# Kernel optimization log

Hardware: AMD Instinct MI355X
Metric: run time of the kernel (lower is better)

## Reference

```python
import jax, jax.numpy as jnp
import numpy as np

B, N_O, N_Q = 2, 512, 512
POS_DIM, LATENT, HEADS, HEAD_DIM, OUT_DIM = 3, 256, 8, 32, 128
HD = HEADS * HEAD_DIM  # == LATENT here


def _lin(key, fan_in, fan_out):
    return jax.random.normal(key, (fan_in, fan_out), jnp.float32) / np.sqrt(fan_in)


def setup_inputs() -> dict:
    key = jax.random.key(0)
    ks = jax.random.split(key, 12)
    return {
        'h_obs': jax.random.normal(ks[0], (B, N_O, LATENT), jnp.float32),
        'pos_obs': jax.random.uniform(ks[1], (B, N_O, POS_DIM), jnp.float32),
        'pos_query': jax.random.uniform(ks[2], (B, N_Q, POS_DIM), jnp.float32),
        'fw1': _lin(ks[3], LATENT, LATENT), 'fb1': jnp.zeros((LATENT,), jnp.float32),
        'fw2': _lin(ks[4], LATENT, HD), 'fb2': jnp.zeros((HD,), jnp.float32),
        'log_sigma': jnp.zeros((HEADS,), jnp.float32),
        'kw1': _lin(ks[5], POS_DIM * 3, LATENT), 'kb1': jnp.zeros((LATENT,), jnp.float32),
        'kw2': _lin(ks[6], LATENT, HEADS), 'kb2': jnp.zeros((HEADS,), jnp.float32),
        'ow': _lin(ks[7], HD, OUT_DIM), 'ob': jnp.zeros((OUT_DIM,), jnp.float32),
        'vw': _lin(ks[8], HD, OUT_DIM), 'vb': jnp.zeros((OUT_DIM,), jnp.float32),
    }


def reference(h_obs, pos_obs, pos_query, fw1, fb1, fw2, fb2, log_sigma,
              kw1, kb1, kw2, kb2, ow, ob, vw, vb):
    Bv, No, _ = h_obs.shape
    Nq = pos_query.shape[1]
    # feature net -> values [B, H, N_o, D]
    v = jax.nn.relu(h_obs @ fw1 + fb1) @ fw2 + fb2
    v = v.reshape(Bv, No, HEADS, HEAD_DIM).transpose(0, 2, 1, 3)
    # pairwise relative positions [B, Nq, No, P]
    pos_q = pos_query[:, :, None, :]
    pos_o = pos_obs[:, None, :, :]
    rel = pos_q - pos_o
    dist2 = jnp.sum(rel ** 2, axis=-1)  # [B, Nq, No]
    sigma = jnp.exp(log_sigma)[None, :, None, None]
    rbf = jnp.exp(-dist2[:, None] / (sigma ** 2 + 1e-6))  # [B, H, Nq, No]
    # kernel MLP on concatenated pairwise positions [B, Nq, No, 3P] -> [B, H, Nq, No]
    ki = jnp.concatenate([
        jnp.broadcast_to(pos_q, (Bv, Nq, No, POS_DIM)),
        jnp.broadcast_to(pos_o, (Bv, Nq, No, POS_DIM)),
        rel], axis=-1)
    delta = (jax.nn.relu(ki @ kw1 + kb1) @ kw2 + kb2).transpose(0, 3, 1, 2)
    logits = jnp.log(rbf + 1e-8) + delta
    weights = jax.nn.softmax(logits, axis=-1)  # [B, H, Nq, No]
    # weighted mean over observations
    v_mean = jnp.einsum('bhqo,bhod->bhqd', weights, v)  # [B, H, Nq, D]
    h_query = v_mean.transpose(0, 2, 1, 3).reshape(Bv, Nq, HD)
    # weighted variance: sum_o w * (v_o - v_mean)^2
    residual = v[:, :, None, :, :] - v_mean[:, :, :, None, :]  # [B, H, Nq, No, D]
    var = jnp.sum(weights[..., None] * residual ** 2, axis=3)  # [B, H, Nq, D]
    var = var.transpose(0, 2, 1, 3).reshape(Bv, Nq, HD)
    mean = h_query @ ow + ob
    var_out = jax.nn.softplus(var @ vw + vb)
    return (mean, var_out)
```

## Files before the change

kernel.cpp:

```cpp
#include <hip/hip_runtime.h>
#include <math.h>

#define NB 2
#define NO 512
#define NQ 512
#define OUT_DIM 128
#define LPAD 514

typedef __attribute__((ext_vector_type(8))) short short8;
typedef __attribute__((ext_vector_type(8))) _Float16 half8;
typedef __attribute__((ext_vector_type(4))) float f32x4;
typedef float v2f __attribute__((ext_vector_type(2)));

__device__ __forceinline__ float softplus_f(float x) {
  return x > 0.0f ? x + log1pf(expf(-x)) : log1pf(expf(x));
}
__device__ __forceinline__ unsigned short bf16_rne(float f) {
  unsigned u = __float_as_uint(f);
  unsigned r = u + 0x7FFFu + ((u >> 16) & 1u);
  return (unsigned short)(r >> 16);
}
__device__ __forceinline__ v2f unpk_bf2(unsigned u) {
  v2f r; r.x = __uint_as_float(u << 16); r.y = __uint_as_float(u & 0xFFFF0000u);
  return r;
}
__device__ __forceinline__ v2f splat2(float x) { v2f r; r.x = x; r.y = x; return r; }
__device__ __forceinline__ v2f fma2(v2f a, v2f b, v2f c) { return __builtin_elementwise_fma(a, b, c); }
__device__ __forceinline__ v2f max2(v2f a, v2f b) { return __builtin_elementwise_max(a, b); }
__device__ __forceinline__ int cvt2h(float x, float y) {
  return __builtin_bit_cast(int, __builtin_amdgcn_cvt_pkrtz(x, y));
}
__device__ __forceinline__ v2f bfly_s(v2f x) {
  #pragma unroll
  for (int off = 8; off <= 32; off <<= 1) {
    x.x += __shfl_xor(x.x, off, 64);
    x.y += __shfl_xor(x.y, off, 64);
  }
  return x;
}

__global__ __launch_bounds__(1024) void prep_kernel(
    const float* __restrict__ h_obs, const float* __restrict__ fw1,
    const float* __restrict__ fb1, const float* __restrict__ fw2,
    const float* __restrict__ fb2, const float* __restrict__ pos_obs,
    const float* __restrict__ kw1, unsigned short* __restrict__ V_bf,
    unsigned short* __restrict__ AO_bf)
{
  if (blockIdx.x < 256) {
    __shared__ float s_red[4][4][256];
    __shared__ float s_hid[4][256];
    const int n  = threadIdx.x & 255;
    const int ks = threadIdx.x >> 8;
    const int r0 = blockIdx.x * 4;
    const int k0 = ks * 64;
    float a0 = 0.f, a1 = 0.f, a2 = 0.f, a3 = 0.f;
    #pragma unroll 8
    for (int kk = 0; kk < 64; ++kk) {
      int k = k0 + kk;
      float w = fw1[k * 256 + n];
      a0 = fmaf(h_obs[(r0 + 0) * 256 + k], w, a0);
      a1 = fmaf(h_obs[(r0 + 1) * 256 + k], w, a1);
      a2 = fmaf(h_obs[(r0 + 2) * 256 + k], w, a2);
      a3 = fmaf(h_obs[(r0 + 3) * 256 + k], w, a3);
    }
    s_red[ks][0][n] = a0; s_red[ks][1][n] = a1;
    s_red[ks][2][n] = a2; s_red[ks][3][n] = a3;
    __syncthreads();
    if (ks == 0) {
      float bb = fb1[n];
      #pragma unroll
      for (int r = 0; r < 4; ++r) {
        float v = s_red[0][r][n] + s_red[1][r][n] + s_red[2][r][n] + s_red[3][r][n] + bb;
        s_hid[r][n] = fmaxf(v, 0.f);
      }
    }
    __syncthreads();
    float c0 = 0.f, c1 = 0.f, c2 = 0.f, c3 = 0.f;
    #pragma unroll 8
    for (int kk = 0; kk < 64; ++kk) {
      int k = k0 + kk;
      float w = fw2[k * 256 + n];
      c0 = fmaf(s_hid[0][k], w, c0);
      c1 = fmaf(s_hid[1][k], w, c1);
      c2 = fmaf(s_hid[2][k], w, c2);
      c3 = fmaf(s_hid[3][k], w, c3);
    }
    __syncthreads();
    s_red[ks][0][n] = c0; s_red[ks][1][n] = c1;
    s_red[ks][2][n] = c2; s_red[ks][3][n] = c3;
    __syncthreads();
    if (ks == 0) {
      float bb = fb2[n];
      #pragma unroll
      for (int r = 0; r < 4; ++r) {
        float v = s_red[0][r][n] + s_red[1][r][n] + s_red[2][r][n] + s_red[3][r][n] + bb;
        V_bf[(size_t)(r0 + r) * 256 + n] = bf16_rne(v);
      }
    }
  } else {
    const int i  = blockIdx.x - 256;
    const int b  = i >> 7;
    const int og = i & 127;
    const int ol = threadIdx.x >> 8;
    const int j  = threadIdx.x & 255;
    const int o  = og * 4 + ol;
    float c0 = kw1[3 * 256 + j] - kw1[6 * 256 + j];
    float c1 = kw1[4 * 256 + j] - kw1[7 * 256 + j];
    float c2 = kw1[5 * 256 + j] - kw1[8 * 256 + j];
    const float* p = pos_obs + ((size_t)(b * NO + o)) * 3;
    AO_bf[(size_t)(b * NO + o) * 256 + j] =
        bf16_rne(fmaf(p[0], c0, fmaf(p[1], c1, p[2] * c2)));
  }
}

__global__ __launch_bounds__(512, 4) void attn_fused(
    const unsigned short* __restrict__ V_bf,
    const unsigned short* __restrict__ AO_bf,
    const float* __restrict__ kw1,
    const float* __restrict__ kb1,
    const float* __restrict__ kw2,
    const float* __restrict__ kb2,
    const float* __restrict__ log_sigma,
    const float* __restrict__ pos_obs,
    const float* __restrict__ pos_query,
    const float* __restrict__ ow, const float* __restrict__ obias,
    const float* __restrict__ vw, const float* __restrict__ vbias,
    float* __restrict__ out)
{
  __shared__ float s_logits[2][8 * LPAD];
  __shared__ half8 s_Bh[512];
  __shared__ __align__(16) float s_pool[2048];
  __shared__ float s_sum[2][8];

  float* s_aq   = s_pool;
  float* s_hv   = s_pool;
  float* s_pred = s_pool + 1024;

  const int t   = threadIdx.x;
  const int bq0 = blockIdx.x * 2;
  const int b   = bq0 >> 9;

  float pqx[2], pqy[2], pqz[2];
  #pragma unroll
  for (int q = 0; q < 2; ++q) {
    pqx[q] = pos_query[(bq0 + q) * 3 + 0];
    pqy[q] = pos_query[(bq0 + q) * 3 + 1];
    pqz[q] = pos_query[(bq0 + q) * 3 + 2];
  }
  {
    const int q = t >> 8, j = t & 255;
    float c0 = kw1[0 * 256 + j] + kw1[6 * 256 + j];
    float c1 = kw1[1 * 256 + j] + kw1[7 * 256 + j];
    float c2 = kw1[2 * 256 + j] + kw1[8 * 256 + j];
    s_aq[q * 256 + j] =
        fmaf(pqx[q], c0, fmaf(pqy[q], c1, fmaf(pqz[q], c2, kb1[j])));
  }
  {
    const int o = t;
    const float* p = pos_obs + (size_t)(b * NO + o) * 3;
    float px = p[0], py = p[1], pz = p[2];
    float d2q[2];
    #pragma unroll
    for (int q = 0; q < 2; ++q) {
      float r0 = pqx[q] - px, r1 = pqy[q] - py, r2 = pqz[q] - pz;
      d2q[q] = r0 * r0 + r1 * r1 + r2 * r2;
    }
    #pragma unroll
    for (int h = 0; h < 8; ++h) {
      float sg  = __expf(log_sigma[h]);
      float inv = 1.0f / (sg * sg + 1e-6f);
      float kbv = kb2[h];
      s_logits[0][h * LPAD + o] = __logf(__expf(-d2q[0] * inv) + 1e-8f) + kbv;
      s_logits[1][h * LPAD + o] = __logf(__expf(-d2q[1] * inv) + 1e-8f) + kbv;
    }
  }
  {
    const int kstep = t >> 6, lane = t & 63;
    const int nh = lane & 15;
    const int kb_ = kstep * 32 + ((lane >> 4) & 3) * 8;
    half8 b8;
    #pragma unroll
    for (int i = 0; i < 8; ++i) {
      float v = (nh < 8) ? kw2[(kb_ + i) * 8 + nh] : 0.f;
      b8[i] = (_Float16)v;
    }
    s_Bh[kstep * 64 + lane] = b8;
  }
  __syncthreads();

  {
    const int wave = t >> 6, lane = t & 63;
    const int quad = lane >> 4, mrow = lane & 15;
    const int tb   = wave * 4;
    f32x4 C[2][4];
    #pragma unroll
    for (int q = 0; q < 2; ++q)
      #pragma unroll
      for (int jt = 0; jt < 4; ++jt) C[q][jt] = (f32x4){0.f, 0.f, 0.f, 0.f};

    for (int kstep = 0; kstep < 8; ++kstep) {
      const int koff = kstep * 32 + quad * 8;
      const v2f* aqp0 = (const v2f*)(s_aq + koff);
      const v2f* aqp1 = (const v2f*)(s_aq + 256 + koff);
      v2f aq0[4], aq1[4];
      #pragma unroll
      for (int i = 0; i < 4; ++i) { aq0[i] = aqp0[i]; aq1[i] = aqp1[i]; }
      half8 bh = s_Bh[kstep * 64 + lane];
      #pragma unroll
      for (int jt = 0; jt < 4; ++jt) {
        const int o = (tb + jt) * 16 + mrow;
        int4 u = *(const int4*)(AO_bf + ((b * NO + o) << 8) + koff);
        v2f ao0 = unpk_bf2((unsigned)u.x), ao1 = unpk_bf2((unsigned)u.y);
        v2f ao2 = unpk_bf2((unsigned)u.z), ao3 = unpk_bf2((unsigned)u.w);
        v2f z = splat2(0.f);
        int4 af0, af1;
        {
          v2f h0 = max2(aq0[0] + ao0, z), h1 = max2(aq0[1] + ao1, z);
          v2f h2 = max2(aq0[2] + ao2, z), h3 = max2(aq0[3] + ao3, z);
          af0.x = cvt2h(h0.x, h0.y); af0.y = cvt2h(h1.x, h1.y);
          af0.z = cvt2h(h2.x, h2.y); af0.w = cvt2h(h3.x, h3.y);
        }
        {
          v2f h0 = max2(aq1[0] + ao0, z), h1 = max2(aq1[1] + ao1, z);
          v2f h2 = max2(aq1[2] + ao2, z), h3 = max2(aq1[3] + ao3, z);
          af1.x = cvt2h(h0.x, h0.y); af1.y = cvt2h(h1.x, h1.y);
          af1.z = cvt2h(h2.x, h2.y); af1.w = cvt2h(h3.x, h3.y);
        }
        half8 a0 = __builtin_bit_cast(half8, af0);
        half8 a1 = __builtin_bit_cast(half8, af1);
        C[0][jt] = __builtin_amdgcn_mfma_f32_16x16x32_f16(a0, bh, C[0][jt], 0, 0, 0);
        C[1][jt] = __builtin_amdgcn_mfma_f32_16x16x32_f16(a1, bh, C[1][jt], 0, 0, 0);
      }
    }
    const int hh = lane & 15;
    if (hh < 8) {
      #pragma unroll
      for (int q = 0; q < 2; ++q)
        #pragma unroll
        for (int jt = 0; jt < 4; ++jt) {
          const int ob2 = (tb + jt) * 16 + quad * 4;
          #pragma unroll
          for (int r = 0; r < 4; ++r)
            s_logits[q][hh * LPAD + ob2 + r] += C[q][jt][r];
        }
    }
  }
  __syncthreads();

  {
    const int wave = t >> 6, lane = t & 63;
    #pragma unroll
    for (int cc = 0; cc < 2; ++cc) {
      const int c = wave * 2 + cc;
      const int q = c >> 3, h = c & 7;
      float* pl = &s_logits[q][h * LPAD];
      float l[8];
      float m = -1e30f;
      #pragma unroll
      for (int k = 0; k < 8; ++k) {
        l[k] = pl[k * 64 + lane];
        m = fmaxf(m, l[k]);
      }
      #pragma unroll
      for (int off = 32; off >= 1; off >>= 1) m = fmaxf(m, __shfl_xor(m, off, 64));
      float s = 0.f;
      #pragma unroll
      for (int k = 0; k < 8; ++k) {
        float p = __expf(l[k] - m);
        pl[k * 64 + lane] = p;
        s += p;
      }
      #pragma unroll
      for (int off = 32; off >= 1; off >>= 1) s += __shfl_xor(s, off, 64);
      if (lane == 0) s_sum[q][h] = s;
    }
  }
  __syncthreads();

  {
    const int h  = t >> 6;
    const int l  = t & 63;
    const int s5 = l >> 3;
    const int dg = l & 7;
    const unsigned short* vb_ = V_bf + ((b * NO) << 8) + h * 32 + dg * 4;
    const float* P0 = &s_logits[0][h * LPAD];
    const float* P1 = &s_logits[1][h * LPAD];
    v2f A0 = splat2(0.f), B0 = A0, C0 = A0, D0 = A0;
    v2f A1 = A0, B1 = A0, C1 = A0, D1 = A0;
    const int ob = s5 * 64, rot = s5 * 8;
    #pragma unroll 4
    for (int oi = 0; oi < 64; oi += 2) {
      const int oo = ob + ((oi + rot) & 63);
      v2f p0 = *(const v2f*)(P0 + oo);
      v2f p1 = *(const v2f*)(P1 + oo);
      uint2 v0 = *(const uint2*)(vb_ + (oo << 8));
      uint2 v1 = *(const uint2*)(vb_ + ((oo + 1) << 8));
      v2f va0 = unpk_bf2(v0.x), vb0 = unpk_bf2(v0.y);
      v2f va1 = unpk_bf2(v1.x), vb1 = unpk_bf2(v1.y);
      v2f t0, t1;
      v2f p00 = splat2(p0.x), p10 = splat2(p1.x);
      A0 = fma2(p00, va0, A0); B0 = fma2(p00, vb0, B0);
      t0 = p00 * va0; C0 = fma2(t0, va0, C0);
      t1 = p00 * vb0; D0 = fma2(t1, vb0, D0);
      A1 = fma2(p10, va0, A1); B1 = fma2(p10, vb0, B1);
      t0 = p10 * va0; C1 = fma2(t0, va0, C1);
      t1 = p10 * vb0; D1 = fma2(t1, vb0, D1);
      v2f p01 = splat2(p0.y), p11 = splat2(p1.y);
      A0 = fma2(p01, va1, A0); B0 = fma2(p01, vb1, B0);
      t0 = p01 * va1; C0 = fma2(t0, va1, C0);
      t1 = p01 * vb1; D0 = fma2(t1, vb1, D0);
      A1 = fma2(p11, va1, A1); B1 = fma2(p11, vb1, B1);
      t0 = p11 * va1; C1 = fma2(t0, va1, C1);
      t1 = p11 * vb1; D1 = fma2(t1, vb1, D1);
    }
    A0 = bfly_s(A0); B0 = bfly_s(B0); C0 = bfly_s(C0); D0 = bfly_s(D0);
    A1 = bfly_s(A1); B1 = bfly_s(B1); C1 = bfly_s(C1); D1 = bfly_s(D1);
    if (s5 < 4) {
      const int q = s5 >> 1, kind = s5 & 1;
      v2f S1a = q ? A1 : A0, S1b = q ? B1 : B0;
      v2f S2a = q ? C1 : C0, S2b = q ? D1 : D0;
      float inv = 1.0f / s_sum[q][h];
      float m0 = S1a.x * inv, m1 = S1a.y * inv;
      float m2 = S1b.x * inv, m3 = S1b.y * inv;
      float4 w;
      if (kind == 0) {
        w = (float4){m0, m1, m2, m3};
      } else {
        w = (float4){fmaxf(S2a.x * inv - m0 * m0, 0.f),
                     fmaxf(S2a.y * inv - m1 * m1, 0.f),
                     fmaxf(S2b.x * inv - m2 * m2, 0.f),
                     fmaxf(S2b.y * inv - m3 * m3, 0.f)};
      }
      *(float4*)(s_hv + (q * 2 + kind) * 256 + h * 32 + dg * 4) = w;
    }
  }
  __syncthreads();

  {
    const int ks = t >> 8, mode = (t >> 7) & 1, n = t & 127;
    const float* W  = mode ? vw : ow;
    const float* X0 = s_hv + mode * 256;
    const float* X1 = s_hv + (2 + mode) * 256;
    float a0 = 0.f, a1 = 0.f;
    const int k0 = ks * 128;
    #pragma unroll 4
    for (int k = k0; k < k0 + 128; k += 4) {
      float4 x0 = *(const float4*)&X0[k];
      float4 x1 = *(const float4*)&X1[k];
      float w0 = W[(k + 0) * 128 + n];
      float w1 = W[(k + 1) * 128 + n];
      float w2 = W[(k + 2) * 128 + n];
      float w3 = W[(k + 3) * 128 + n];
      a0 = fmaf(x0.x, w0, a0); a1 = fmaf(x1.x, w0, a1);
      a0 = fmaf(x0.y, w1, a0); a1 = fmaf(x1.y, w1, a1);
      a0 = fmaf(x0.z, w2, a0); a1 = fmaf(x1.z, w2, a1);
      a0 = fmaf(x0.w, w3, a0); a1 = fmaf(x1.w, w3, a1);
    }
    s_pred[((ks * 2 + mode) * 2 + 0) * 128 + n] = a0;
    s_pred[((ks * 2 + mode) * 2 + 1) * 128 + n] = a1;
  }
  __syncthreads();
  {
    const int q = t >> 8, mode = (t >> 7) & 1, n = t & 127;
    float v = s_pred[((0 * 2 + mode) * 2 + q) * 128 + n]
            + s_pred[((1 * 2 + mode) * 2 + q) * 128 + n]
            + (mode ? vbias[n] : obias[n]);
    if (mode) v = softplus_f(v);
    out[(size_t)mode * (NB * NQ * OUT_DIM) + (size_t)(bq0 + q) * OUT_DIM + n] = v;
  }
}

extern "C" void kernel_launch(void* const* d_in, const int* in_sizes, int n_in,
                              void* d_out, int out_size, void* d_ws, size_t ws_size,
                              hipStream_t stream)
{
  const float* h_obs     = (const float*)d_in[0];
  const float* pos_obs   = (const float*)d_in[1];
  const float* pos_query = (const float*)d_in[2];
  const float* fw1       = (const float*)d_in[3];
  const float* fb1       = (const float*)d_in[4];
  const float* fw2       = (const float*)d_in[5];
  const float* fb2       = (const float*)d_in[6];
  const float* log_sigma = (const float*)d_in[7];
  const float* kw1       = (const float*)d_in[8];
  const float* kb1       = (const float*)d_in[9];
  const float* kw2       = (const float*)d_in[10];
  const float* kb2       = (const float*)d_in[11];
  const float* ow        = (const float*)d_in[12];
  const float* ob        = (const float*)d_in[13];
  const float* vw        = (const float*)d_in[14];
  const float* vb        = (const float*)d_in[15];

  float* out = (float*)d_out;
  unsigned short* ws = (unsigned short*)d_ws;

  unsigned short* V_bf  = ws;
  unsigned short* AO_bf = ws + 262144;

  prep_kernel<<<512, 1024, 0, stream>>>(h_obs, fw1, fb1, fw2, fb2,
                                        pos_obs, kw1, V_bf, AO_bf);
  attn_fused<<<NB * NQ / 2, 512, 0, stream>>>(V_bf, AO_bf, kw1, kb1, kw2, kb2,
                                              log_sigma, pos_obs, pos_query,
                                              ow, ob, vw, vb, out);
}
```

Measured before the change: 139.5 us.

## Move weighted mean/variance reduction onto MFMA with transposed fp16 V and V²

The prep kernel now writes V and V² in fp16, transposed per head as [b,h,d,o], and writes the AO table in fp16 instead of bf16. The attention kernel computes the kernel-MLP hidden layer with packed fp16 add/max, removing the bf16 unpack and convert steps. It replaces the scalar FMA loop for weighted sums (with butterfly reductions) by MFMA 16x16x32 ops over the softmax probabilities. The softmax is merged into the same per-head block, which removes a barrier and s_sum. The cost is fp16 precision for V² and for the probabilities, plus extra workspace for VT2, and most MFMA output columns are unused since only two queries are live per tile.

```diff
diff --git a/kernel.cpp b/kernel.cpp
--- a/kernel.cpp
+++ b/kernel.cpp
@@ -5,46 +5,27 @@
 #define NO 512
 #define NQ 512
 #define OUT_DIM 128
-#define LPAD 514
-
-typedef __attribute__((ext_vector_type(8))) short short8;
+#define LPAD 516
+
 typedef __attribute__((ext_vector_type(8))) _Float16 half8;
+typedef __attribute__((ext_vector_type(4))) _Float16 half4;
 typedef __attribute__((ext_vector_type(4))) float f32x4;
-typedef float v2f __attribute__((ext_vector_type(2)));
 
 __device__ __forceinline__ float softplus_f(float x) {
   return x > 0.0f ? x + log1pf(expf(-x)) : log1pf(expf(x));
 }
-__device__ __forceinline__ unsigned short bf16_rne(float f) {
-  unsigned u = __float_as_uint(f);
-  unsigned r = u + 0x7FFFu + ((u >> 16) & 1u);
-  return (unsigned short)(r >> 16);
-}
-__device__ __forceinline__ v2f unpk_bf2(unsigned u) {
-  v2f r; r.x = __uint_as_float(u << 16); r.y = __uint_as_float(u & 0xFFFF0000u);
-  return r;
-}
-__device__ __forceinline__ v2f splat2(float x) { v2f r; r.x = x; r.y = x; return r; }
-__device__ __forceinline__ v2f fma2(v2f a, v2f b, v2f c) { return __builtin_elementwise_fma(a, b, c); }
-__device__ __forceinline__ v2f max2(v2f a, v2f b) { return __builtin_elementwise_max(a, b); }
 __device__ __forceinline__ int cvt2h(float x, float y) {
   return __builtin_bit_cast(int, __builtin_amdgcn_cvt_pkrtz(x, y));
-}
-__device__ __forceinline__ v2f bfly_s(v2f x) {
-  #pragma unroll
-  for (int off = 8; off <= 32; off <<= 1) {
-    x.x += __shfl_xor(x.x, off, 64);
-    x.y += __shfl_xor(x.y, off, 64);
-  }
-  return x;
 }
 
 __global__ __launch_bounds__(1024) void prep_kernel(
     const float* __restrict__ h_obs, const float* __restrict__ fw1,
     const float* __restrict__ fb1, const float* __restrict__ fw2,
     const float* __restrict__ fb2, const float* __restrict__ pos_obs,
-    const float* __restrict__ kw1, unsigned short* __restrict__ V_bf,
-    unsigned short* __restrict__ AO_bf)
+    const float* __restrict__ kw1,
+    _Float16* __restrict__ VT,
+    _Float16* __restrict__ VT2,
+    _Float16* __restrict__ AO_h)
 {
   if (blockIdx.x < 256) {
     __shared__ float s_red[4][4][256];
@@ -91,11 +72,21 @@
     __syncthreads();
     if (ks == 0) {
       float bb = fb2[n];
+      float vr[4];
+      #pragma unroll
+      for (int r = 0; r < 4; ++r)
+        vr[r] = s_red[0][r][n] + s_red[1][r][n] + s_red[2][r][n] + s_red[3][r][n] + bb;
+      const int h  = n >> 5, d = n & 31;
+      const int bb_ = r0 >> 9, o0 = r0 & 511;
+      half4 pv, pv2;
       #pragma unroll
       for (int r = 0; r < 4; ++r) {
-        float v = s_red[0][r][n] + s_red[1][r][n] + s_red[2][r][n] + s_red[3][r][n] + bb;
-        V_bf[(size_t)(r0 + r) * 256 + n] = bf16_rne(v);
-      }
+        pv[r]  = (_Float16)vr[r];
+        pv2[r] = (_Float16)(vr[r] * vr[r]);
+      }
+      const size_t idx = ((size_t)((bb_ * 8 + h) * 32 + d)) * 512 + o0;
+      *(half4*)(VT  + idx) = pv;
+      *(half4*)(VT2 + idx) = pv2;
     }
   } else {
     const int i  = blockIdx.x - 256;
@@ -108,14 +99,15 @@
     float c1 = kw1[4 * 256 + j] - kw1[7 * 256 + j];
     float c2 = kw1[5 * 256 + j] - kw1[8 * 256 + j];
     const float* p = pos_obs + ((size_t)(b * NO + o)) * 3;
-    AO_bf[(size_t)(b * NO + o) * 256 + j] =
-        bf16_rne(fmaf(p[0], c0, fmaf(p[1], c1, p[2] * c2)));
+    AO_h[(size_t)(b * NO + o) * 256 + j] =
+        (_Float16)(fmaf(p[0], c0, fmaf(p[1], c1, p[2] * c2)));
   }
 }
 
 __global__ __launch_bounds__(512, 4) void attn_fused(
-    const unsigned short* __restrict__ V_bf,
-    const unsigned short* __restrict__ AO_bf,
+    const _Float16* __restrict__ VT,
+    const _Float16* __restrict__ VT2,
+    const _Float16* __restrict__ AO_h,
     const float* __restrict__ kw1,
     const float* __restrict__ kb1,
     const float* __restrict__ kw2,
@@ -127,14 +119,13 @@
     const float* __restrict__ vw, const float* __restrict__ vbias,
     float* __restrict__ out)
 {
-  __shared__ float s_logits[2][8 * LPAD];
+  __shared__ __align__(16) float s_logits[2][8 * LPAD];
   __shared__ half8 s_Bh[512];
   __shared__ __align__(16) float s_pool[2048];
-  __shared__ float s_sum[2][8];
-
-  float* s_aq   = s_pool;
-  float* s_hv   = s_pool;
-  float* s_pred = s_pool + 1024;
+
+  _Float16* s_aq2 = (_Float16*)s_pool;
+  float*    s_hv  = s_pool;
+  float*    s_pred = s_pool + 1024;
 
   const int t   = threadIdx.x;
   const int bq0 = blockIdx.x * 2;
@@ -152,7 +143,7 @@
     float c0 = kw1[0 * 256 + j] + kw1[6 * 256 + j];
     float c1 = kw1[1 * 256 + j] + kw1[7 * 256 + j];
     float c2 = kw1[2 * 256 + j] + kw1[8 * 256 + j];
-    s_aq[q * 256 + j] =
+    s_aq2[q * 256 + j] = (_Float16)
         fmaf(pqx[q], c0, fmaf(pqy[q], c1, fmaf(pqz[q], c2, kb1[j])));
   }
   {
@@ -198,36 +189,18 @@
       #pragma unroll
       for (int jt = 0; jt < 4; ++jt) C[q][jt] = (f32x4){0.f, 0.f, 0.f, 0.f};
 
+    const half8 z8 = {0, 0, 0, 0, 0, 0, 0, 0};
     for (int kstep = 0; kstep < 8; ++kstep) {
       const int koff = kstep * 32 + quad * 8;
-      const v2f* aqp0 = (const v2f*)(s_aq + koff);
-      const v2f* aqp1 = (const v2f*)(s_aq + 256 + koff);
-      v2f aq0[4], aq1[4];
-      #pragma unroll
-      for (int i = 0; i < 4; ++i) { aq0[i] = aqp0[i]; aq1[i] = aqp1[i]; }
-      half8 bh = s_Bh[kstep * 64 + lane];
+      half8 aq0 = *(const half8*)(s_aq2 + koff);
+      half8 aq1 = *(const half8*)(s_aq2 + 256 + koff);
+      half8 bh  = s_Bh[kstep * 64 + lane];
       #pragma unroll
       for (int jt = 0; jt < 4; ++jt) {
         const int o = (tb + jt) * 16 + mrow;
-        int4 u = *(const int4*)(AO_bf + ((b * NO + o) << 8) + koff);
-        v2f ao0 = unpk_bf2((unsigned)u.x), ao1 = unpk_bf2((unsigned)u.y);
-        v2f ao2 = unpk_bf2((unsigned)u.z), ao3 = unpk_bf2((unsigned)u.w);
-        v2f z = splat2(0.f);
-        int4 af0, af1;
-        {
-          v2f h0 = max2(aq0[0] + ao0, z), h1 = max2(aq0[1] + ao1, z);
-          v2f h2 = max2(aq0[2] + ao2, z), h3 = max2(aq0[3] + ao3, z);
-          af0.x = cvt2h(h0.x, h0.y); af0.y = cvt2h(h1.x, h1.y);
-          af0.z = cvt2h(h2.x, h2.y); af0.w = cvt2h(h3.x, h3.y);
-        }
-        {
-          v2f h0 = max2(aq1[0] + ao0, z), h1 = max2(aq1[1] + ao1, z);
-          v2f h2 = max2(aq1[2] + ao2, z), h3 = max2(aq1[3] + ao3, z);
-          af1.x = cvt2h(h0.x, h0.y); af1.y = cvt2h(h1.x, h1.y);
-          af1.z = cvt2h(h2.x, h2.y); af1.w = cvt2h(h3.x, h3.y);
-        }
-        half8 a0 = __builtin_bit_cast(half8, af0);
-        half8 a1 = __builtin_bit_cast(half8, af1);
+        half8 ao = *(const half8*)(AO_h + ((size_t)(b * NO + o) << 8) + koff);
+        half8 a0 = __builtin_elementwise_max(aq0 + ao, z8);
+        half8 a1 = __builtin_elementwise_max(aq1 + ao, z8);
         C[0][jt] = __builtin_amdgcn_mfma_f32_16x16x32_f16(a0, bh, C[0][jt], 0, 0, 0);
         C[1][jt] = __builtin_amdgcn_mfma_f32_16x16x32_f16(a1, bh, C[1][jt], 0, 0, 0);
       }
@@ -248,90 +221,70 @@
   __syncthreads();
 
   {
-    const int wave = t >> 6, lane = t & 63;
-    #pragma unroll
-    for (int cc = 0; cc < 2; ++cc) {
-      const int c = wave * 2 + cc;
-      const int q = c >> 3, h = c & 7;
+    const int h = t >> 6, lane = t & 63;
+    float invq[2];
+    #pragma unroll
+    for (int q = 0; q < 2; ++q) {
       float* pl = &s_logits[q][h * LPAD];
-      float l[8];
+      float l8[8];
       float m = -1e30f;
       #pragma unroll
       for (int k = 0; k < 8; ++k) {
-        l[k] = pl[k * 64 + lane];
-        m = fmaxf(m, l[k]);
+        l8[k] = pl[k * 64 + lane];
+        m = fmaxf(m, l8[k]);
       }
       #pragma unroll
       for (int off = 32; off >= 1; off >>= 1) m = fmaxf(m, __shfl_xor(m, off, 64));
       float s = 0.f;
       #pragma unroll
       for (int k = 0; k < 8; ++k) {
-        float p = __expf(l[k] - m);
+        float p = __expf(l8[k] - m);
         pl[k * 64 + lane] = p;
         s += p;
       }
       #pragma unroll
       for (int off = 32; off >= 1; off >>= 1) s += __shfl_xor(s, off, 64);
-      if (lane == 0) s_sum[q][h] = s;
-    }
-  }
-  __syncthreads();
-
-  {
-    const int h  = t >> 6;
-    const int l  = t & 63;
-    const int s5 = l >> 3;
-    const int dg = l & 7;
-    const unsigned short* vb_ = V_bf + ((b * NO) << 8) + h * 32 + dg * 4;
-    const float* P0 = &s_logits[0][h * LPAD];
-    const float* P1 = &s_logits[1][h * LPAD];
-    v2f A0 = splat2(0.f), B0 = A0, C0 = A0, D0 = A0;
-    v2f A1 = A0, B1 = A0, C1 = A0, D1 = A0;
-    const int ob = s5 * 64, rot = s5 * 8;
+      invq[q] = 1.0f / s;
+    }
+    const int nq = lane & 15, kg = lane >> 4, dl = lane & 15;
+    const size_t vbase = ((size_t)(b * 8 + h) * 32 + dl) * 512;
+    const _Float16* vt1 = VT  + vbase;
+    const _Float16* vt2 = VT2 + vbase;
+    const float* P = &s_logits[nq & 1][h * LPAD];
+    f32x4 Cm0 = {0.f,0.f,0.f,0.f}, Cm1 = Cm0, Cv0 = Cm0, Cv1 = Cm0;
     #pragma unroll 4
-    for (int oi = 0; oi < 64; oi += 2) {
-      const int oo = ob + ((oi + rot) & 63);
-      v2f p0 = *(const v2f*)(P0 + oo);
-      v2f p1 = *(const v2f*)(P1 + oo);
-      uint2 v0 = *(const uint2*)(vb_ + (oo << 8));
-      uint2 v1 = *(const uint2*)(vb_ + ((oo + 1) << 8));
-      v2f va0 = unpk_bf2(v0.x), vb0 = unpk_bf2(v0.y);
-      v2f va1 = unpk_bf2(v1.x), vb1 = unpk_bf2(v1.y);
-      v2f t0, t1;
-      v2f p00 = splat2(p0.x), p10 = splat2(p1.x);
-      A0 = fma2(p00, va0, A0); B0 = fma2(p00, vb0, B0);
-      t0 = p00 * va0; C0 = fma2(t0, va0, C0);
-      t1 = p00 * vb0; D0 = fma2(t1, vb0, D0);
-      A1 = fma2(p10, va0, A1); B1 = fma2(p10, vb0, B1);
-      t0 = p10 * va0; C1 = fma2(t0, va0, C1);
-      t1 = p10 * vb0; D1 = fma2(t1, vb0, D1);
-      v2f p01 = splat2(p0.y), p11 = splat2(p1.y);
-      A0 = fma2(p01, va1, A0); B0 = fma2(p01, vb1, B0);
-      t0 = p01 * va1; C0 = fma2(t0, va1, C0);
-      t1 = p01 * vb1; D0 = fma2(t1, vb1, D0);
-      A1 = fma2(p11, va1, A1); B1 = fma2(p11, vb1, B1);
-      t0 = p11 * va1; C1 = fma2(t0, va1, C1);
-      t1 = p11 * vb1; D1 = fma2(t1, vb1, D1);
-    }
-    A0 = bfly_s(A0); B0 = bfly_s(B0); C0 = bfly_s(C0); D0 = bfly_s(D0);
-    A1 = bfly_s(A1); B1 = bfly_s(B1); C1 = bfly_s(C1); D1 = bfly_s(D1);
-    if (s5 < 4) {
-      const int q = s5 >> 1, kind = s5 & 1;
-      v2f S1a = q ? A1 : A0, S1b = q ? B1 : B0;
-      v2f S2a = q ? C1 : C0, S2b = q ? D1 : D0;
-      float inv = 1.0f / s_sum[q][h];
-      float m0 = S1a.x * inv, m1 = S1a.y * inv;
-      float m2 = S1b.x * inv, m3 = S1b.y * inv;
-      float4 w;
-      if (kind == 0) {
-        w = (float4){m0, m1, m2, m3};
-      } else {
-        w = (float4){fmaxf(S2a.x * inv - m0 * m0, 0.f),
-                     fmaxf(S2a.y * inv - m1 * m1, 0.f),
-                     fmaxf(S2b.x * inv - m2 * m2, 0.f),
-                     fmaxf(S2b.y * inv - m3 * m3, 0.f)};
-      }
-      *(float4*)(s_hv + (q * 2 + kind) * 256 + h * 32 + dg * 4) = w;
+    for (int ks = 0; ks < 16; ++ks) {
+      const int ob = ks * 32 + kg * 8;
+      float4 p0 = *(const float4*)(P + ob);
+      float4 p1 = *(const float4*)(P + ob + 4);
+      int4 bi;
+      bi.x = cvt2h(p0.x, p0.y); bi.y = cvt2h(p0.z, p0.w);
+      bi.z = cvt2h(p1.x, p1.y); bi.w = cvt2h(p1.z, p1.w);
+      half8 bh = __builtin_bit_cast(half8, bi);
+      half8 am0 = *(const half8*)(vt1 + ob);
+      half8 am1 = *(const half8*)(vt1 + 8192 + ob);
+      half8 av0 = *(const half8*)(vt2 + ob);
+      half8 av1 = *(const half8*)(vt2 + 8192 + ob);
+      Cm0 = __builtin_amdgcn_mfma_f32_16x16x32_f16(am0, bh, Cm0, 0, 0, 0);
+      Cm1 = __builtin_amdgcn_mfma_f32_16x16x32_f16(am1, bh, Cm1, 0, 0, 0);
+      Cv0 = __builtin_amdgcn_mfma_f32_16x16x32_f16(av0, bh, Cv0, 0, 0, 0);
+      Cv1 = __builtin_amdgcn_mfma_f32_16x16x32_f16(av1, bh, Cv1, 0, 0, 0);
+    }
+    if (nq < 2) {
+      const float iv = nq ? invq[1] : invq[0];
+      const int dbase = h * 32 + kg * 4;
+      f32x4 m0, v0, m1, v1;
+      #pragma unroll
+      for (int r = 0; r < 4; ++r) {
+        float a = Cm0[r] * iv;
+        m0[r] = a; v0[r] = fmaxf(Cv0[r] * iv - a * a, 0.f);
+        float c = Cm1[r] * iv;
+        m1[r] = c; v1[r] = fmaxf(Cv1[r] * iv - c * c, 0.f);
+      }
+      *(f32x4*)(s_hv + (nq * 2 + 0) * 256 + dbase)      = m0;
+      *(f32x4*)(s_hv + (nq * 2 + 1) * 256 + dbase)      = v0;
+      *(f32x4*)(s_hv + (nq * 2 + 0) * 256 + dbase + 16) = m1;
+      *(f32x4*)(s_hv + (nq * 2 + 1) * 256 + dbase + 16) = v1;
     }
   }
   __syncthreads();
@@ -392,14 +345,15 @@
   const float* vb        = (const float*)d_in[15];
 
   float* out = (float*)d_out;
-  unsigned short* ws = (unsigned short*)d_ws;
-
-  unsigned short* V_bf  = ws;
-  unsigned short* AO_bf = ws + 262144;
+  _Float16* ws = (_Float16*)d_ws;
+
+  _Float16* AO_h = ws;
+  _Float16* VT   = ws + 262144;
+  _Float16* VT2  = ws + 524288;
 
   prep_kernel<<<512, 1024, 0, stream>>>(h_obs, fw1, fb1, fw2, fb2,
-                                        pos_obs, kw1, V_bf, AO_bf);
-  attn_fused<<<NB * NQ / 2, 512, 0, stream>>>(V_bf, AO_bf, kw1, kb1, kw2, kb2,
+                                        pos_obs, kw1, VT, VT2, AO_h);
+  attn_fused<<<NB * NQ / 2, 512, 0, stream>>>(VT, VT2, AO_h, kw1, kb1, kw2, kb2,
                                               log_sigma, pos_obs, pos_query,
                                               ow, ob, vw, vb, out);
 }
```

Measured after the change: 155.2 us. +11.3%, slower.
